# Kernel optimization log

Hardware: AMD Instinct MI355X
Metric: run time of the kernel (lower is better)

The kernel has to match this reference:

```python
import jax, jax.numpy as jnp
import numpy as np


def setup_inputs() -> dict:
    key = jax.random.key(0)
    k1, k2 = jax.random.split(key)
    N, P, T, H, W = 8, 32, 16, 384, 384
    # binary {0,1} masks, stored as float32 (original binarizes via bool().long())
    groups_pred = jax.random.randint(k1, (N, P, H, W), 0, 2).astype(jnp.float32)
    groups_true = jax.random.randint(k2, (N, T, H, W), 0, 2).astype(jnp.float32)
    return {"groups_pred": groups_pred, "groups_true": groups_true}


def reference(groups_pred, groups_true):
    # Binarize (matches .bool().long() in the original)
    Gp = (groups_pred != 0).astype(jnp.float32)  # (N,P,H,W)
    Gt = (groups_true != 0).astype(jnp.float32)  # (N,T,H,W)

    # Pairwise intersection as a batched contraction over H,W --
    # avoids materializing the (N,P,T,H,W) broadcast tensor.
    inter = jnp.einsum('nphw,nthw->npt', Gp, Gt)  # (N,P,T)

    # For binary masks: |Gp ∪ Gt| = |Gp| + |Gt| - |Gp ∩ Gt|
    area_p = Gp.sum(axis=(-2, -1))  # (N,P)
    area_t = Gt.sum(axis=(-2, -1))  # (N,T)
    union = area_p[:, :, None] + area_t[:, None, :] - inter  # (N,P,T)

    # ious with 0/0 -> 0 (original sets non-finite entries to 0)
    safe_union = jnp.where(union > 0, union, 1.0)
    ious = jnp.where(union > 0, inter / safe_union, 0.0)  # (N,P,T)

    iou_max = ious.max(axis=-1)  # (N,P): best-matching true segment per pred

    # Weighted per-pixel sum of best-IoU over predicted masks, normalized by coverage
    num = jnp.einsum('np,nphw->nhw', iou_max, Gp)  # (N,H,W)
    den = Gp.sum(axis=1)                            # (N,H,W)
    score = jnp.where(den > 0, num / jnp.where(den > 0, den, 1.0), 0.0)
    return score
```

## Files before the change

### kernel.cpp

```cpp
#include <hip/hip_runtime.h>
#include <cstdint>
#include <cstddef>

typedef unsigned long long u64;

constexpr int N_  = 8;
constexpr int P_  = 32;
constexpr int T_  = 16;
constexpr int HW  = 384 * 384;
constexpr int WORDS = HW / 64;
constexpr int GPN = HW / 256;

__global__ void pack_kernel(const float* __restrict__ src, u64* __restrict__ dst,
                            int ngroups) {
    int wave   = (blockIdx.x * blockDim.x + threadIdx.x) >> 6;
    int lane   = threadIdx.x & 63;
    int nwaves = (gridDim.x * blockDim.x) >> 6;
    for (int g = wave; g < ngroups; g += nwaves) {
        float4 v = reinterpret_cast<const float4*>(src)[(size_t)g * 64 + lane];
        u64 b0 = __ballot(v.x != 0.0f);
        u64 b1 = __ballot(v.y != 0.0f);
        u64 b2 = __ballot(v.z != 0.0f);
        u64 b3 = __ballot(v.w != 0.0f);
        if (lane == 0) {
            u64* d = dst + (size_t)g * 4;
            d[0] = b0; d[1] = b1; d[2] = b2; d[3] = b3;
        }
    }
}

__device__ inline int block_reduce_sum(int v) {
    __shared__ int buf[4];
    #pragma unroll
    for (int o = 32; o >= 1; o >>= 1) v += __shfl_down(v, o, 64);
    __syncthreads();
    if ((threadIdx.x & 63) == 0) buf[threadIdx.x >> 6] = v;
    __syncthreads();
    return buf[0] + buf[1] + buf[2] + buf[3];
}

__global__ __launch_bounds__(256)
void inter_kernel(const u64* __restrict__ pp, const u64* __restrict__ pt,
                  float* __restrict__ inter, float* __restrict__ area_p,
                  float* __restrict__ area_t) {
    const int np = blockIdx.x;
    const int n  = np >> 5;
    const int p  = np & 31;
    const int tid = threadIdx.x;

    const u64* pw = pp + (size_t)np * WORDS;
    u64 a[9];
    #pragma unroll
    for (int k = 0; k < 9; ++k) a[k] = pw[tid + 256 * k];

    int my_area = 0;
    #pragma unroll
    for (int k = 0; k < 9; ++k) my_area += __popcll(a[k]);
    int ap = block_reduce_sum(my_area);
    if (tid == 0) area_p[np] = (float)ap;

    for (int t = 0; t < T_; ++t) {
        const u64* tw = pt + ((size_t)(n * T_ + t)) * WORDS;
        int s = 0, st = 0;
        #pragma unroll
        for (int k = 0; k < 9; ++k) {
            u64 w = tw[tid + 256 * k];
            s += __popcll(a[k] & w);
            if (p == 0) st += __popcll(w);
        }
        int is = block_reduce_sum(s);
        if (tid == 0) inter[(size_t)np * T_ + t] = (float)is;
        if (p == 0) {
            int at = block_reduce_sum(st);
            if (tid == 0) area_t[n * T_ + t] = (float)at;
        }
    }
}

__global__ __launch_bounds__(256)
void score_kernel(const u64* __restrict__ pm,
                  const float* __restrict__ inter,
                  const float* __restrict__ area_p,
                  const float* __restrict__ area_t,
                  float* __restrict__ out) {
    __shared__ u64   wlds[P_][16];
    __shared__ float iou[P_];

    const int tid  = threadIdx.x;
    const int lane = tid & 63;
    const int wv   = tid >> 6;
    const int gblk = blockIdx.x * 4;
    const int n    = gblk / GPN;
    const int gl0  = gblk - n * GPN;

    {
        int p = tid >> 3, k = tid & 7;
        const u64* s = pm + ((size_t)(n * P_ + p)) * WORDS + (size_t)gl0 * 4 + 2 * k;
        ulonglong2 v = *reinterpret_cast<const ulonglong2*>(s);
        *reinterpret_cast<ulonglong2*>(&wlds[p][2 * k]) = v;
    }

    if (tid < P_) {
        float ap = area_p[n * P_ + tid];
        float best = 0.0f;
        #pragma unroll
        for (int t = 0; t < T_; ++t) {
            float it = inter[(size_t)(n * P_ + tid) * T_ + t];
            float u  = ap + area_t[n * T_ + t] - it;
            best = fmaxf(best, (u > 0.0f) ? it / u : 0.0f);
        }
        iou[tid] = best;
    }
    __syncthreads();

    float num0 = 0.f, num1 = 0.f, num2 = 0.f, num3 = 0.f;
    int   den0 = 0, den1 = 0, den2 = 0, den3 = 0;
    #pragma unroll
    for (int p = 0; p < P_; ++p) {
        float w8 = iou[p];
        u64 w0 = wlds[p][wv * 4 + 0];
        u64 w1 = wlds[p][wv * 4 + 1];
        u64 w2 = wlds[p][wv * 4 + 2];
        u64 w3 = wlds[p][wv * 4 + 3];
        unsigned b0 = (unsigned)(w0 >> lane) & 1u;
        unsigned b1 = (unsigned)(w1 >> lane) & 1u;
        unsigned b2 = (unsigned)(w2 >> lane) & 1u;
        unsigned b3 = (unsigned)(w3 >> lane) & 1u;
        num0 += b0 ? w8 : 0.0f;  den0 += b0;
        num1 += b1 ? w8 : 0.0f;  den1 += b1;
        num2 += b2 ? w8 : 0.0f;  den2 += b2;
        num3 += b3 ? w8 : 0.0f;  den3 += b3;
    }

    float4 o;
    o.x = den0 ? num0 / (float)den0 : 0.0f;
    o.y = den1 ? num1 / (float)den1 : 0.0f;
    o.z = den2 ? num2 / (float)den2 : 0.0f;
    o.w = den3 ? num3 / (float)den3 : 0.0f;
    reinterpret_cast<float4*>(out)[(size_t)(gblk + wv) * 64 + lane] = o;
}

extern "C" void kernel_launch(void* const* d_in, const int* in_sizes, int n_in,
                              void* d_out, int out_size, void* d_ws, size_t ws_size,
                              hipStream_t stream) {
    const float* gp = (const float*)d_in[0];
    const float* gt = (const float*)d_in[1];
    float* out = (float*)d_out;

    char* ws = (char*)d_ws;
    u64*   packed_p = (u64*)ws;
    u64*   packed_t = (u64*)(ws + (size_t)N_ * P_ * WORDS * 8);
    float* inter    = (float*)(ws + (size_t)(N_ * P_ + N_ * T_) * WORDS * 8);
    float* area_p   = inter + N_ * P_ * T_;
    float* area_t   = area_p + N_ * P_;

    const int pred_groups = N_ * P_ * HW / 256;
    const int true_groups = N_ * T_ * HW / 256;

    hipLaunchKernelGGL(pack_kernel, dim3(2048), dim3(256), 0, stream, gp, packed_p, pred_groups);
    hipLaunchKernelGGL(pack_kernel, dim3(1024), dim3(256), 0, stream, gt, packed_t, true_groups);
    hipLaunchKernelGGL(inter_kernel, dim3(N_ * P_), dim3(256), 0, stream,
                       packed_p, packed_t, inter, area_p, area_t);
    hipLaunchKernelGGL(score_kernel, dim3(N_ * GPN / 4), dim3(256), 0, stream,
                       packed_p, inter, area_p, area_t, out);
}
```

Baseline: 78.96 us.

## Fuse mask packing with intersection counting using shared-memory tiles and atomics

Replaces the two pack kernels and the separate intersection kernel with one kernel. Each block binarizes a small spatial chunk of all pred and true masks for one batch, keeps the bit words in shared memory, and computes pairwise popcount intersections and areas there. Partial counts are accumulated into zeroed integer buffers with atomics, and only the pred bitmasks are written out for the score kernel. This removes the packed-true round trip and the serialized 16-step per-block reduction loop, at the cost of a memset, many atomics and two block barriers per chunk.

```diff
diff --git a/kernel.cpp b/kernel.cpp
--- a/kernel.cpp
+++ b/kernel.cpp
@@ -10,78 +10,84 @@
 constexpr int HW  = 384 * 384;
 constexpr int WORDS = HW / 64;
 constexpr int GPN = HW / 256;
-
-__global__ void pack_kernel(const float* __restrict__ src, u64* __restrict__ dst,
-                            int ngroups) {
-    int wave   = (blockIdx.x * blockDim.x + threadIdx.x) >> 6;
-    int lane   = threadIdx.x & 63;
-    int nwaves = (gridDim.x * blockDim.x) >> 6;
-    for (int g = wave; g < ngroups; g += nwaves) {
-        float4 v = reinterpret_cast<const float4*>(src)[(size_t)g * 64 + lane];
-        u64 b0 = __ballot(v.x != 0.0f);
-        u64 b1 = __ballot(v.y != 0.0f);
-        u64 b2 = __ballot(v.z != 0.0f);
-        u64 b3 = __ballot(v.w != 0.0f);
-        if (lane == 0) {
-            u64* d = dst + (size_t)g * 4;
-            d[0] = b0; d[1] = b1; d[2] = b2; d[3] = b3;
-        }
-    }
-}
-
-__device__ inline int block_reduce_sum(int v) {
-    __shared__ int buf[4];
-    #pragma unroll
-    for (int o = 32; o >= 1; o >>= 1) v += __shfl_down(v, o, 64);
-    __syncthreads();
-    if ((threadIdx.x & 63) == 0) buf[threadIdx.x >> 6] = v;
-    __syncthreads();
-    return buf[0] + buf[1] + buf[2] + buf[3];
-}
+constexpr int M_  = P_ + T_;
+constexpr int CHUNK = 6;
+constexpr int BPN = GPN / CHUNK;
 
 __global__ __launch_bounds__(256)
-void inter_kernel(const u64* __restrict__ pp, const u64* __restrict__ pt,
-                  float* __restrict__ inter, float* __restrict__ area_p,
-                  float* __restrict__ area_t) {
-    const int np = blockIdx.x;
-    const int n  = np >> 5;
-    const int p  = np & 31;
-    const int tid = threadIdx.x;
+void fused_pack_inter(const float* __restrict__ gp, const float* __restrict__ gt,
+                      u64* __restrict__ pp, int* __restrict__ inter,
+                      int* __restrict__ area) {
+    __shared__ __align__(16) u64 words[M_][6];
 
-    const u64* pw = pp + (size_t)np * WORDS;
-    u64 a[9];
-    #pragma unroll
-    for (int k = 0; k < 9; ++k) a[k] = pw[tid + 256 * k];
+    const int tid  = threadIdx.x;
+    const int lane = tid & 63;
+    const int wv   = tid >> 6;
+    const int n    = blockIdx.x / BPN;
+    const int g0   = (blockIdx.x - n * BPN) * CHUNK;
 
-    int my_area = 0;
-    #pragma unroll
-    for (int k = 0; k < 9; ++k) my_area += __popcll(a[k]);
-    int ap = block_reduce_sum(my_area);
-    if (tid == 0) area_p[np] = (float)ap;
+    const int p  = tid >> 3;
+    const int t0 = (tid & 7) * 2;
+    const int t1 = t0 + 1;
 
-    for (int t = 0; t < T_; ++t) {
-        const u64* tw = pt + ((size_t)(n * T_ + t)) * WORDS;
-        int s = 0, st = 0;
+    int acc0 = 0, acc1 = 0;
+    int areaAcc[12] = {};
+
+    for (int c = 0; c < CHUNK; ++c) {
+        const int g = g0 + c;
         #pragma unroll
-        for (int k = 0; k < 9; ++k) {
-            u64 w = tw[tid + 256 * k];
-            s += __popcll(a[k] & w);
-            if (p == 0) st += __popcll(w);
+        for (int k = 0; k < 12; ++k) {
+            const int m = wv * 12 + k;
+            const float* src = (m < P_)
+                ? gp + (size_t)(n * P_ + m) * HW
+                : gt + (size_t)(n * T_ + (m - P_)) * HW;
+            float4 v = reinterpret_cast<const float4*>(src + (size_t)g * 256)[lane];
+            u64 b0 = __ballot(v.x != 0.0f);
+            u64 b1 = __ballot(v.y != 0.0f);
+            u64 b2 = __ballot(v.z != 0.0f);
+            u64 b3 = __ballot(v.w != 0.0f);
+            areaAcc[k] += __popcll(b0) + __popcll(b1) + __popcll(b2) + __popcll(b3);
+            if (lane == 0) {
+                ulonglong2 w01, w23;
+                w01.x = b0; w01.y = b1; w23.x = b2; w23.y = b3;
+                *reinterpret_cast<ulonglong2*>(&words[m][0]) = w01;
+                *reinterpret_cast<ulonglong2*>(&words[m][2]) = w23;
+                if (m < P_) {
+                    u64* d = pp + (size_t)(n * P_ + m) * WORDS + (size_t)g * 4;
+                    *reinterpret_cast<ulonglong2*>(d)     = w01;
+                    *reinterpret_cast<ulonglong2*>(d + 2) = w23;
+                }
+            }
         }
-        int is = block_reduce_sum(s);
-        if (tid == 0) inter[(size_t)np * T_ + t] = (float)is;
-        if (p == 0) {
-            int at = block_reduce_sum(st);
-            if (tid == 0) area_t[n * T_ + t] = (float)at;
+        __syncthreads();
+        {
+            ulonglong2 a01 = *reinterpret_cast<const ulonglong2*>(&words[p][0]);
+            ulonglong2 a23 = *reinterpret_cast<const ulonglong2*>(&words[p][2]);
+            ulonglong2 b01 = *reinterpret_cast<const ulonglong2*>(&words[P_ + t0][0]);
+            ulonglong2 b23 = *reinterpret_cast<const ulonglong2*>(&words[P_ + t0][2]);
+            ulonglong2 c01 = *reinterpret_cast<const ulonglong2*>(&words[P_ + t1][0]);
+            ulonglong2 c23 = *reinterpret_cast<const ulonglong2*>(&words[P_ + t1][2]);
+            acc0 += __popcll(a01.x & b01.x) + __popcll(a01.y & b01.y)
+                  + __popcll(a23.x & b23.x) + __popcll(a23.y & b23.y);
+            acc1 += __popcll(a01.x & c01.x) + __popcll(a01.y & c01.y)
+                  + __popcll(a23.x & c23.x) + __popcll(a23.y & c23.y);
         }
+        __syncthreads();
+    }
+
+    atomicAdd(&inter[(n * P_ + p) * T_ + t0], acc0);
+    atomicAdd(&inter[(n * P_ + p) * T_ + t1], acc1);
+    if (lane == 0) {
+        #pragma unroll
+        for (int k = 0; k < 12; ++k)
+            atomicAdd(&area[n * M_ + wv * 12 + k], areaAcc[k]);
     }
 }
 
 __global__ __launch_bounds__(256)
 void score_kernel(const u64* __restrict__ pm,
-                  const float* __restrict__ inter,
-                  const float* __restrict__ area_p,
-                  const float* __restrict__ area_t,
+                  const int* __restrict__ inter,
+                  const int* __restrict__ area,
                   float* __restrict__ out) {
     __shared__ u64   wlds[P_][16];
     __shared__ float iou[P_];
@@ -95,18 +101,18 @@
 
     {
         int p = tid >> 3, k = tid & 7;
-        const u64* s = pm + ((size_t)(n * P_ + p)) * WORDS + (size_t)gl0 * 4 + 2 * k;
-        ulonglong2 v = *reinterpret_cast<const ulonglong2*>(s);
-        *reinterpret_cast<ulonglong2*>(&wlds[p][2 * k]) = v;
+        const u64* s = pm + (size_t)(n * P_ + p) * WORDS + (size_t)gl0 * 4 + 2 * k;
+        *reinterpret_cast<ulonglong2*>(&wlds[p][2 * k]) =
+            *reinterpret_cast<const ulonglong2*>(s);
     }
 
     if (tid < P_) {
-        float ap = area_p[n * P_ + tid];
+        float ap = (float)area[n * M_ + tid];
         float best = 0.0f;
         #pragma unroll
         for (int t = 0; t < T_; ++t) {
-            float it = inter[(size_t)(n * P_ + tid) * T_ + t];
-            float u  = ap + area_t[n * T_ + t] - it;
+            float it = (float)inter[(n * P_ + tid) * T_ + t];
+            float u  = ap + (float)area[n * M_ + P_ + t] - it;
             best = fmaxf(best, (u > 0.0f) ? it / u : 0.0f);
         }
         iou[tid] = best;
@@ -148,19 +154,14 @@
     float* out = (float*)d_out;
 
     char* ws = (char*)d_ws;
-    u64*   packed_p = (u64*)ws;
-    u64*   packed_t = (u64*)(ws + (size_t)N_ * P_ * WORDS * 8);
-    float* inter    = (float*)(ws + (size_t)(N_ * P_ + N_ * T_) * WORDS * 8);
-    float* area_p   = inter + N_ * P_ * T_;
-    float* area_t   = area_p + N_ * P_;
+    int* inter = (int*)ws;
+    int* area  = (int*)(ws + 16384);
+    u64* packed_p = (u64*)(ws + 16384 + 1536);
 
-    const int pred_groups = N_ * P_ * HW / 256;
-    const int true_groups = N_ * T_ * HW / 256;
+    hipMemsetAsync(ws, 0, 16384 + 1536, stream);
 
-    hipLaunchKernelGGL(pack_kernel, dim3(2048), dim3(256), 0, stream, gp, packed_p, pred_groups);
-    hipLaunchKernelGGL(pack_kernel, dim3(1024), dim3(256), 0, stream, gt, packed_t, true_groups);
-    hipLaunchKernelGGL(inter_kernel, dim3(N_ * P_), dim3(256), 0, stream,
-                       packed_p, packed_t, inter, area_p, area_t);
+    hipLaunchKernelGGL(fused_pack_inter, dim3(N_ * BPN), dim3(256), 0, stream,
+                       gp, gt, packed_p, inter, area);
     hipLaunchKernelGGL(score_kernel, dim3(N_ * GPN / 4), dim3(256), 0, stream,
-                       packed_p, inter, area_p, area_t, out);
+                       packed_p, inter, area, out);
 }
```

Result: slower. 106.4 us (+34.7%).

## Merge pack launches, batch block reductions, compute IoU max in intersection kernel

Applied to the files above, without the earlier changes.

Merges the two pack launches into one grid-stride kernel that covers both pred and true masks. The intersection kernel now keeps all 33 partial counts in registers and reduces them in one pass with a single barrier phase, instead of syncing after every true mask. It also computes the per-pred IoU max itself, so the score kernel only reads one float per pred. This cuts launch count, barriers, and score-kernel prologue work, at the cost of every block recomputing true-mask areas and holding more registers.

```diff
diff --git a/kernel.cpp b/kernel.cpp
--- a/kernel.cpp
+++ b/kernel.cpp
@@ -10,78 +10,101 @@
 constexpr int HW  = 384 * 384;
 constexpr int WORDS = HW / 64;
 constexpr int GPN = HW / 256;
+constexpr int PG  = N_ * P_ * HW / 256;
+constexpr int TG  = N_ * T_ * HW / 256;
 
-__global__ void pack_kernel(const float* __restrict__ src, u64* __restrict__ dst,
-                            int ngroups) {
+__global__ __launch_bounds__(256)
+void pack_all(const float* __restrict__ gp, const float* __restrict__ gt,
+              u64* __restrict__ pp, u64* __restrict__ pt) {
     int wave   = (blockIdx.x * blockDim.x + threadIdx.x) >> 6;
     int lane   = threadIdx.x & 63;
     int nwaves = (gridDim.x * blockDim.x) >> 6;
-    for (int g = wave; g < ngroups; g += nwaves) {
-        float4 v = reinterpret_cast<const float4*>(src)[(size_t)g * 64 + lane];
+    for (int g = wave; g < PG + TG; g += nwaves) {
+        const float4* src;
+        u64* dst;
+        if (g < PG) { src = reinterpret_cast<const float4*>(gp) + (size_t)g * 64;
+                      dst = pp + (size_t)g * 4; }
+        else        { src = reinterpret_cast<const float4*>(gt) + (size_t)(g - PG) * 64;
+                      dst = pt + (size_t)(g - PG) * 4; }
+        float4 v = src[lane];
         u64 b0 = __ballot(v.x != 0.0f);
         u64 b1 = __ballot(v.y != 0.0f);
         u64 b2 = __ballot(v.z != 0.0f);
         u64 b3 = __ballot(v.w != 0.0f);
-        if (lane == 0) {
-            u64* d = dst + (size_t)g * 4;
-            d[0] = b0; d[1] = b1; d[2] = b2; d[3] = b3;
-        }
+        if (lane == 0) { dst[0] = b0; dst[1] = b1; dst[2] = b2; dst[3] = b3; }
     }
 }
 
-__device__ inline int block_reduce_sum(int v) {
-    __shared__ int buf[4];
-    #pragma unroll
-    for (int o = 32; o >= 1; o >>= 1) v += __shfl_down(v, o, 64);
-    __syncthreads();
-    if ((threadIdx.x & 63) == 0) buf[threadIdx.x >> 6] = v;
-    __syncthreads();
-    return buf[0] + buf[1] + buf[2] + buf[3];
-}
+__global__ __launch_bounds__(256)
+void ioumax_kernel(const u64* __restrict__ pp, const u64* __restrict__ pt,
+                   float* __restrict__ ioumax) {
+    __shared__ int   red[4][33];
+    __shared__ int   tot[33];
+    __shared__ float shiou[T_];
 
-__global__ __launch_bounds__(256)
-void inter_kernel(const u64* __restrict__ pp, const u64* __restrict__ pt,
-                  float* __restrict__ inter, float* __restrict__ area_p,
-                  float* __restrict__ area_t) {
-    const int np = blockIdx.x;
-    const int n  = np >> 5;
-    const int p  = np & 31;
+    const int np  = blockIdx.x;
+    const int n   = np >> 5;
     const int tid = threadIdx.x;
+    const int lane = tid & 63;
+    const int wv   = tid >> 6;
 
     const u64* pw = pp + (size_t)np * WORDS;
     u64 a[9];
     #pragma unroll
     for (int k = 0; k < 9; ++k) a[k] = pw[tid + 256 * k];
 
-    int my_area = 0;
+    int vals[33];
+    {
+        int ap = 0;
+        #pragma unroll
+        for (int k = 0; k < 9; ++k) ap += __popcll(a[k]);
+        vals[0] = ap;
+    }
     #pragma unroll
-    for (int k = 0; k < 9; ++k) my_area += __popcll(a[k]);
-    int ap = block_reduce_sum(my_area);
-    if (tid == 0) area_p[np] = (float)ap;
-
     for (int t = 0; t < T_; ++t) {
-        const u64* tw = pt + ((size_t)(n * T_ + t)) * WORDS;
+        const u64* tw = pt + (size_t)(n * T_ + t) * WORDS;
         int s = 0, st = 0;
         #pragma unroll
         for (int k = 0; k < 9; ++k) {
             u64 w = tw[tid + 256 * k];
-            s += __popcll(a[k] & w);
-            if (p == 0) st += __popcll(w);
+            s  += __popcll(a[k] & w);
+            st += __popcll(w);
         }
-        int is = block_reduce_sum(s);
-        if (tid == 0) inter[(size_t)np * T_ + t] = (float)is;
-        if (p == 0) {
-            int at = block_reduce_sum(st);
-            if (tid == 0) area_t[n * T_ + t] = (float)at;
-        }
+        vals[1 + t]       = s;
+        vals[1 + T_ + t]  = st;
+    }
+
+    #pragma unroll
+    for (int i = 0; i < 33; ++i) {
+        int v = vals[i];
+        v += __shfl_down(v, 32);
+        v += __shfl_down(v, 16);
+        v += __shfl_down(v, 8);
+        v += __shfl_down(v, 4);
+        v += __shfl_down(v, 2);
+        v += __shfl_down(v, 1);
+        if (lane == 0) red[wv][i] = v;
+    }
+    __syncthreads();
+    if (tid < 33) tot[tid] = red[0][tid] + red[1][tid] + red[2][tid] + red[3][tid];
+    __syncthreads();
+    if (tid < T_) {
+        float it = (float)tot[1 + tid];
+        float u  = (float)tot[0] + (float)tot[1 + T_ + tid] - it;
+        shiou[tid] = (u > 0.0f) ? it / u : 0.0f;
+    }
+    __syncthreads();
+    if (tid == 0) {
+        float best = 0.0f;
+        #pragma unroll
+        for (int t = 0; t < T_; ++t) best = fmaxf(best, shiou[t]);
+        ioumax[np] = best;
     }
 }
 
 __global__ __launch_bounds__(256)
 void score_kernel(const u64* __restrict__ pm,
-                  const float* __restrict__ inter,
-                  const float* __restrict__ area_p,
-                  const float* __restrict__ area_t,
+                  const float* __restrict__ ioumax,
                   float* __restrict__ out) {
     __shared__ u64   wlds[P_][16];
     __shared__ float iou[P_];
@@ -95,22 +118,11 @@
 
     {
         int p = tid >> 3, k = tid & 7;
-        const u64* s = pm + ((size_t)(n * P_ + p)) * WORDS + (size_t)gl0 * 4 + 2 * k;
-        ulonglong2 v = *reinterpret_cast<const ulonglong2*>(s);
-        *reinterpret_cast<ulonglong2*>(&wlds[p][2 * k]) = v;
+        const u64* s = pm + (size_t)(n * P_ + p) * WORDS + (size_t)gl0 * 4 + 2 * k;
+        *reinterpret_cast<ulonglong2*>(&wlds[p][2 * k]) =
+            *reinterpret_cast<const ulonglong2*>(s);
     }
-
-    if (tid < P_) {
-        float ap = area_p[n * P_ + tid];
-        float best = 0.0f;
-        #pragma unroll
-        for (int t = 0; t < T_; ++t) {
-            float it = inter[(size_t)(n * P_ + tid) * T_ + t];
-            float u  = ap + area_t[n * T_ + t] - it;
-            best = fmaxf(best, (u > 0.0f) ? it / u : 0.0f);
-        }
-        iou[tid] = best;
-    }
+    if (tid < P_) iou[tid] = ioumax[n * P_ + tid];
     __syncthreads();
 
     float num0 = 0.f, num1 = 0.f, num2 = 0.f, num3 = 0.f;
@@ -148,19 +160,14 @@
     float* out = (float*)d_out;
 
     char* ws = (char*)d_ws;
-    u64*   packed_p = (u64*)ws;
-    u64*   packed_t = (u64*)(ws + (size_t)N_ * P_ * WORDS * 8);
-    float* inter    = (float*)(ws + (size_t)(N_ * P_ + N_ * T_) * WORDS * 8);
-    float* area_p   = inter + N_ * P_ * T_;
-    float* area_t   = area_p + N_ * P_;
+    u64* packed_p = (u64*)ws;
+    u64* packed_t = (u64*)(ws + (size_t)N_ * P_ * WORDS * 8);
+    float* ioumax = (float*)(ws + (size_t)(N_ * P_ + N_ * T_) * WORDS * 8);
 
-    const int pred_groups = N_ * P_ * HW / 256;
-    const int true_groups = N_ * T_ * HW / 256;
-
-    hipLaunchKernelGGL(pack_kernel, dim3(2048), dim3(256), 0, stream, gp, packed_p, pred_groups);
-    hipLaunchKernelGGL(pack_kernel, dim3(1024), dim3(256), 0, stream, gt, packed_t, true_groups);
-    hipLaunchKernelGGL(inter_kernel, dim3(N_ * P_), dim3(256), 0, stream,
-                       packed_p, packed_t, inter, area_p, area_t);
+    hipLaunchKernelGGL(pack_all, dim3(2048), dim3(256), 0, stream,
+                       gp, gt, packed_p, packed_t);
+    hipLaunchKernelGGL(ioumax_kernel, dim3(N_ * P_), dim3(256), 0, stream,
+                       packed_p, packed_t, ioumax);
     hipLaunchKernelGGL(score_kernel, dim3(N_ * GPN / 4), dim3(256), 0, stream,
-                       packed_p, inter, area_p, area_t, out);
+                       packed_p, ioumax, out);
 }
```

Result: faster. 73.21 us (-7.3%).
